# Optimization experiments

Measured on AMD Instinct MI355X. Metric: run time of the kernel, lower is better.

The kernel has to match this reference:

```python
import jax, jax.numpy as jnp
import numpy as np

S, B, E, H = 2048, 2, 1024, 16
D = E // H  # head dim = 64


def setup_inputs() -> dict:
    key = jax.random.key(0)
    k1, k2, k3 = jax.random.split(key, 3)
    x = jax.random.normal(k1, (S, B, E), dtype=jnp.float32)
    Wqkv = jax.random.normal(k2, (3 * E, E), dtype=jnp.float32) * (E ** -0.5)
    bqkv = jax.random.normal(k3, (3 * E,), dtype=jnp.float32) * 0.02
    return {"x": x, "Wqkv": Wqkv, "bqkv": bqkv}


def reference(x, Wqkv, bqkv):
    s, b, e = x.shape
    h, d = H, E // H
    # fused QKV projection: [S,B,E] @ [E,3E] -> [S,B,3E]
    qkv = jnp.einsum('sbe,fe->sbf', x, Wqkv) + bqkv
    q, k, v = jnp.split(qkv, 3, axis=-1)
    q = q.reshape(s, b, h, d)
    k = k.reshape(s, b, h, d)
    v = v.reshape(s, b, h, d)
    scale = 1.0 / jnp.sqrt(jnp.asarray(d, dtype=x.dtype))
    # scores: [B,H,S,S]
    scores = jnp.einsum('sbhd,tbhd->bhst', q, k) * scale
    attn = jax.nn.softmax(scores, axis=-1)
    # context: [S,B,H,D] -> [S,B,E]
    ctx = jnp.einsum('bhst,tbhd->sbhd', attn, v)
    return ctx.reshape(s, b, e)
```

## Files before the change

### kernel.cpp

```cpp
#include <hip/hip_runtime.h>

constexpr int SEQ   = 2048;
constexpr int BATCH = 2;
constexpr int EMB   = 1024;
constexpr int NH    = 16;
constexpr int HDIM  = 64;
constexpr int MROWS = SEQ * BATCH;
constexpr int KDIM  = EMB;
constexpr int NCOLS = 3 * EMB;

typedef __bf16 bf16x8 __attribute__((ext_vector_type(8)));
typedef __bf16 bf16x4 __attribute__((ext_vector_type(4)));
typedef float  f32x4  __attribute__((ext_vector_type(4)));
typedef float  f32x16 __attribute__((ext_vector_type(16)));
typedef unsigned int u32;
typedef unsigned int u32x4 __attribute__((ext_vector_type(4)));

__device__ __forceinline__ u32 cvt_pk_bf16(float lo, float hi) {
  u32 r;
  asm("v_cvt_pk_bf16_f32 %0, %1, %2" : "=v"(r) : "v"(lo), "v"(hi));
  return r;
}
__device__ __forceinline__ void pl32_swap(u32& a, u32& b) {
  asm("v_permlane32_swap_b32 %0, %1" : "+v"(a), "+v"(b));
}

__global__ __launch_bounds__(256) void cvt_f32_bf16(
    const float* __restrict__ src, __bf16* __restrict__ dst, int n4) {
  int stride = gridDim.x * blockDim.x;
  for (int i = blockIdx.x * blockDim.x + threadIdx.x; i < n4; i += stride) {
    float4 v = reinterpret_cast<const float4*>(src)[i];
    bf16x4 o;
    o[0] = (__bf16)v.x; o[1] = (__bf16)v.y; o[2] = (__bf16)v.z; o[3] = (__bf16)v.w;
    reinterpret_cast<bf16x4*>(dst)[i] = o;
  }
}

__global__ __launch_bounds__(256) void qkv_gemm(
    const __bf16* __restrict__ Xb, const __bf16* __restrict__ Wb,
    const float* __restrict__ bqkv,
    __bf16* __restrict__ Qb, __bf16* __restrict__ Kb, __bf16* __restrict__ Vt) {
  __shared__ __attribute__((aligned(16))) __bf16 Al[128][40];
  __shared__ __attribute__((aligned(16))) __bf16 Bl[128][40];

  const int tid  = threadIdx.x;
  const int lane = tid & 63;
  const int w    = tid >> 6;
  const int wm   = w >> 1, wn = w & 1;
  const int m0   = blockIdx.y * 128;
  const int n0   = blockIdx.x * 128;

  f32x4 acc[4][4] = {};

  for (int kt = 0; kt < KDIM / 32; ++kt) {
    const int k0 = kt * 32;
#pragma unroll
    for (int i = 0; i < 2; ++i) {
      int u = tid + i * 256;
      int row = u >> 2, c = u & 3;
      *reinterpret_cast<bf16x8*>(&Al[row][c * 8]) =
          *reinterpret_cast<const bf16x8*>(&Xb[(size_t)(m0 + row) * KDIM + k0 + c * 8]);
      *reinterpret_cast<bf16x8*>(&Bl[row][c * 8]) =
          *reinterpret_cast<const bf16x8*>(&Wb[(size_t)(n0 + row) * KDIM + k0 + c * 8]);
    }
    __syncthreads();

    bf16x8 af[4], bfr[4];
#pragma unroll
    for (int i = 0; i < 4; ++i)
      af[i] = *reinterpret_cast<const bf16x8*>(&Al[wm * 64 + i * 16 + (lane & 15)][(lane >> 4) * 8]);
#pragma unroll
    for (int j = 0; j < 4; ++j)
      bfr[j] = *reinterpret_cast<const bf16x8*>(&Bl[wn * 64 + j * 16 + (lane & 15)][(lane >> 4) * 8]);
#pragma unroll
    for (int i = 0; i < 4; ++i)
#pragma unroll
      for (int j = 0; j < 4; ++j)
        acc[i][j] = __builtin_amdgcn_mfma_f32_16x16x32_bf16(af[i], bfr[j], acc[i][j], 0, 0, 0);
    __syncthreads();
  }

  const float QSCALE = 0.18033688011112042f;
#pragma unroll
  for (int j = 0; j < 4; ++j) {
    const int f    = n0 + wn * 64 + j * 16 + (lane & 15);
    const float bias = bqkv[f];
    const int sec  = f >> 10;
    const int hd   = f & 1023;
    const int h    = hd >> 6, d = hd & 63;
#pragma unroll
    for (int i = 0; i < 4; ++i) {
#pragma unroll
      for (int r = 0; r < 4; ++r) {
        const int mm = m0 + wm * 64 + i * 16 + (lane >> 4) * 4 + r;
        const int s_ = mm >> 1, b_ = mm & 1;
        const int bh = b_ * NH + h;
        const float val = acc[i][j][r] + bias;
        if (sec == 0) {
          Qb[((size_t)bh * SEQ + s_) * HDIM + d] = (__bf16)(val * QSCALE);
        } else if (sec == 1) {
          Kb[((size_t)bh * SEQ + s_) * HDIM + d] = (__bf16)val;
        } else {
          Vt[((size_t)bh * HDIM + d) * SEQ + s_] = (__bf16)val;
        }
      }
    }
  }
}

__global__ __launch_bounds__(512) void attn_fwd(
    const __bf16* __restrict__ Qb, const __bf16* __restrict__ Kb,
    const __bf16* __restrict__ Vt, float* __restrict__ out) {
  __shared__ __attribute__((aligned(16))) __bf16 lds[8192];
  __bf16* Kl = lds;
  __bf16* Vl = lds + 4096;

  const int tid  = threadIdx.x;
  const int lane = tid & 63;
  const int w    = tid >> 6;
  const int lq   = lane & 31;
  const int hi   = lane >> 5;
  const int bh   = blockIdx.y;
  const int b_   = bh >> 4, h = bh & 15;
  const int q0   = blockIdx.x * 256 + w * 32;

  const __bf16* Qp = Qb + (size_t)bh * SEQ * HDIM;
  const __bf16* Kp = Kb + (size_t)bh * SEQ * HDIM;
  const __bf16* Vp = Vt + (size_t)bh * HDIM * SEQ;

  bf16x8 qf[4];
#pragma unroll
  for (int ks = 0; ks < 4; ++ks)
    qf[ks] = *reinterpret_cast<const bf16x8*>(&Qp[(size_t)(q0 + lq) * HDIM + ks * 16 + hi * 8]);

  f32x16 acc0 = {}, acc1 = {};
  float m = -1e30f, l = 0.f;

  const int srow = tid >> 3;
  const int scol = (tid & 7) * 8;
  const int sidx = srow * 64 + (scol ^ ((srow & 7) << 3));

  for (int t0 = 0; t0 < SEQ; t0 += 64) {
    __syncthreads();
    *reinterpret_cast<bf16x8*>(&Kl[sidx]) =
        *reinterpret_cast<const bf16x8*>(&Kp[(size_t)(t0 + srow) * HDIM + scol]);
    *reinterpret_cast<bf16x8*>(&Vl[sidx]) =
        *reinterpret_cast<const bf16x8*>(&Vp[(size_t)srow * SEQ + t0 + scol]);
    __syncthreads();

    f32x16 S0 = {}, S1 = {};
#pragma unroll
    for (int ks = 0; ks < 4; ++ks) {
      const int colb = ks * 16 + hi * 8;
      bf16x8 k0 = *reinterpret_cast<const bf16x8*>(&Kl[lq * 64        + (colb ^ ((lq & 7) << 3))]);
      bf16x8 k1 = *reinterpret_cast<const bf16x8*>(&Kl[(32 + lq) * 64 + (colb ^ ((lq & 7) << 3))]);
      S0 = __builtin_amdgcn_mfma_f32_32x32x16_bf16(k0, qf[ks], S0, 0, 0, 0);
      S1 = __builtin_amdgcn_mfma_f32_32x32x16_bf16(k1, qf[ks], S1, 0, 0, 0);
    }

    float pmax = S0[0];
#pragma unroll
    for (int i = 1; i < 16; ++i) pmax = fmaxf(pmax, S0[i]);
#pragma unroll
    for (int i = 0; i < 16; ++i) pmax = fmaxf(pmax, S1[i]);
    pmax = fmaxf(pmax, __shfl_xor(pmax, 32));
    const float mnew  = fmaxf(m, pmax);
    const float alpha = __builtin_amdgcn_exp2f(m - mnew);
    m = mnew;
    float rs = 0.f;
#pragma unroll
    for (int i = 0; i < 16; ++i) { S0[i] = __builtin_amdgcn_exp2f(S0[i] - mnew); rs += S0[i]; }
#pragma unroll
    for (int i = 0; i < 16; ++i) { S1[i] = __builtin_amdgcn_exp2f(S1[i] - mnew); rs += S1[i]; }
    l = l * alpha + rs;
#pragma unroll
    for (int i = 0; i < 16; ++i) { acc0[i] *= alpha; acc1[i] *= alpha; }

    bf16x8 pw[4];
    {
      auto mk = [&](const f32x16& P, bf16x8* dst) {
#pragma unroll
        for (int kk = 0; kk < 2; ++kk) {
          u32 a0 = cvt_pk_bf16(P[kk * 8 + 0], P[kk * 8 + 1]);
          u32 b0 = cvt_pk_bf16(P[kk * 8 + 4], P[kk * 8 + 5]);
          u32 a1 = cvt_pk_bf16(P[kk * 8 + 2], P[kk * 8 + 3]);
          u32 b1 = cvt_pk_bf16(P[kk * 8 + 6], P[kk * 8 + 7]);
          pl32_swap(a0, b0);
          pl32_swap(a1, b1);
          u32x4 wv; wv[0] = a0; wv[1] = a1; wv[2] = b0; wv[3] = b1;
          dst[kk] = __builtin_bit_cast(bf16x8, wv);
        }
      };
      mk(S0, &pw[0]);
      mk(S1, &pw[2]);
    }

#pragma unroll
    for (int ks = 0; ks < 4; ++ks) {
      const int colb = ks * 16 + hi * 8;
      bf16x8 v0 = *reinterpret_cast<const bf16x8*>(&Vl[lq * 64        + (colb ^ ((lq & 7) << 3))]);
      bf16x8 v1 = *reinterpret_cast<const bf16x8*>(&Vl[(32 + lq) * 64 + (colb ^ ((lq & 7) << 3))]);
      acc0 = __builtin_amdgcn_mfma_f32_32x32x16_bf16(v0, pw[ks], acc0, 0, 0, 0);
      acc1 = __builtin_amdgcn_mfma_f32_32x32x16_bf16(v1, pw[ks], acc1, 0, 0, 0);
    }
  }

  l += __shfl_xor(l, 32);
  const float inv = 1.0f / l;
  const int s_ = q0 + lq;
  float* op = out + ((size_t)s_ * BATCH + b_) * EMB + h * HDIM;
#pragma unroll
  for (int rr = 0; rr < 4; ++rr) {
    float4 o0 = {acc0[4 * rr] * inv, acc0[4 * rr + 1] * inv,
                 acc0[4 * rr + 2] * inv, acc0[4 * rr + 3] * inv};
    *reinterpret_cast<float4*>(&op[8 * rr + 4 * hi]) = o0;
    float4 o1 = {acc1[4 * rr] * inv, acc1[4 * rr + 1] * inv,
                 acc1[4 * rr + 2] * inv, acc1[4 * rr + 3] * inv};
    *reinterpret_cast<float4*>(&op[8 * rr + 4 * hi + 32]) = o1;
  }
}

extern "C" void kernel_launch(void* const* d_in, const int* in_sizes, int n_in,
                              void* d_out, int out_size, void* d_ws, size_t ws_size,
                              hipStream_t stream) {
  (void)in_sizes; (void)n_in; (void)out_size; (void)ws_size;
  const float* x    = (const float*)d_in[0];
  const float* Wqkv = (const float*)d_in[1];
  const float* bias = (const float*)d_in[2];
  float* out = (float*)d_out;

  char* ws = (char*)d_ws;
  __bf16* Xb = (__bf16*)(ws);
  __bf16* Wb = (__bf16*)(ws + 8388608);
  __bf16* Qb = (__bf16*)(ws + 14680064);
  __bf16* Kb = (__bf16*)(ws + 23068672);
  __bf16* Vt = (__bf16*)(ws + 31457280);

  cvt_f32_bf16<<<dim3(1024), dim3(256), 0, stream>>>(x, Xb, (MROWS * KDIM) / 4);
  cvt_f32_bf16<<<dim3(768), dim3(256), 0, stream>>>(Wqkv, Wb, (NCOLS * KDIM) / 4);
  qkv_gemm<<<dim3(NCOLS / 128, MROWS / 128), dim3(256), 0, stream>>>(Xb, Wb, bias, Qb, Kb, Vt);
  attn_fwd<<<dim3(SEQ / 256, BATCH * NH), dim3(512), 0, stream>>>(Qb, Kb, Vt, out);
}
```

Measured before the change: 117.5 us.

## Use direct global-to-LDS loads, double-buffer attention K/V, remap attention grid

The QKV GEMM now stages X and W tiles with global_load_lds into XOR-swizzled 64-wide K tiles, halving the number of loop iterations and barriers. The attention kernel double-buffers K/V tiles in LDS, prefetching the next tile with direct global-to-LDS loads while computing on the current one. It also switches to 256-thread blocks over a 1D grid of 512 workgroups with a remapped block-to-(head, query-tile) order. The aim is to hide global load latency and remove register round-trips. The cost is more LDS per block. The prefetch relies on a single barrier per iteration to order the async LDS writes, which is a correctness risk if the loads are not waited on.

New measurement: 126.1 us. +7.3%, slower.

```diff
diff --git a/kernel.cpp b/kernel.cpp
--- a/kernel.cpp
+++ b/kernel.cpp
@@ -24,6 +24,11 @@
 __device__ __forceinline__ void pl32_swap(u32& a, u32& b) {
   asm("v_permlane32_swap_b32 %0, %1" : "+v"(a), "+v"(b));
 }
+__device__ __forceinline__ void g2l16(const __bf16* g, __bf16* l) {
+  __builtin_amdgcn_global_load_lds(
+      (const __attribute__((address_space(1))) void*)g,
+      (__attribute__((address_space(3))) void*)l, 16, 0, 0);
+}
 
 __global__ __launch_bounds__(256) void cvt_f32_bf16(
     const float* __restrict__ src, __bf16* __restrict__ dst, int n4) {
@@ -40,8 +45,8 @@
     const __bf16* __restrict__ Xb, const __bf16* __restrict__ Wb,
     const float* __restrict__ bqkv,
     __bf16* __restrict__ Qb, __bf16* __restrict__ Kb, __bf16* __restrict__ Vt) {
-  __shared__ __attribute__((aligned(16))) __bf16 Al[128][40];
-  __shared__ __attribute__((aligned(16))) __bf16 Bl[128][40];
+  __shared__ __attribute__((aligned(16))) __bf16 Al[128 * 64];
+  __shared__ __attribute__((aligned(16))) __bf16 Bl[128 * 64];
 
   const int tid  = threadIdx.x;
   const int lane = tid & 63;
@@ -52,32 +57,36 @@
 
   f32x4 acc[4][4] = {};
 
-  for (int kt = 0; kt < KDIM / 32; ++kt) {
-    const int k0 = kt * 32;
-#pragma unroll
-    for (int i = 0; i < 2; ++i) {
-      int u = tid + i * 256;
-      int row = u >> 2, c = u & 3;
-      *reinterpret_cast<bf16x8*>(&Al[row][c * 8]) =
-          *reinterpret_cast<const bf16x8*>(&Xb[(size_t)(m0 + row) * KDIM + k0 + c * 8]);
-      *reinterpret_cast<bf16x8*>(&Bl[row][c * 8]) =
-          *reinterpret_cast<const bf16x8*>(&Wb[(size_t)(n0 + row) * KDIM + k0 + c * 8]);
-    }
+  for (int kt = 0; kt < KDIM / 64; ++kt) {
+    const int k0 = kt * 64;
     __syncthreads();
-
-    bf16x8 af[4], bfr[4];
-#pragma unroll
-    for (int i = 0; i < 4; ++i)
-      af[i] = *reinterpret_cast<const bf16x8*>(&Al[wm * 64 + i * 16 + (lane & 15)][(lane >> 4) * 8]);
-#pragma unroll
-    for (int j = 0; j < 4; ++j)
-      bfr[j] = *reinterpret_cast<const bf16x8*>(&Bl[wn * 64 + j * 16 + (lane & 15)][(lane >> 4) * 8]);
-#pragma unroll
-    for (int i = 0; i < 4; ++i)
-#pragma unroll
-      for (int j = 0; j < 4; ++j)
-        acc[i][j] = __builtin_amdgcn_mfma_f32_16x16x32_bf16(af[i], bfr[j], acc[i][j], 0, 0, 0);
+#pragma unroll
+    for (int c = 0; c < 4; ++c) {
+      const int u   = (w * 4 + c) * 64 + lane;
+      const int row = u >> 3;
+      const int sc  = ((u & 7) * 8) ^ ((row & 7) << 3);
+      g2l16(&Xb[(size_t)(m0 + row) * KDIM + k0 + sc], Al + (w * 4 + c) * 512);
+      g2l16(&Wb[(size_t)(n0 + row) * KDIM + k0 + sc], Bl + (w * 4 + c) * 512);
+    }
     __syncthreads();
+
+#pragma unroll
+    for (int s = 0; s < 2; ++s) {
+      bf16x8 af[4], bfr[4];
+#pragma unroll
+      for (int i = 0; i < 4; ++i) {
+        const int ra = wm * 64 + i * 16 + (lane & 15);
+        const int rb = wn * 64 + i * 16 + (lane & 15);
+        const int colb = s * 32 + (lane >> 4) * 8;
+        af[i]  = *reinterpret_cast<const bf16x8*>(&Al[ra * 64 + (colb ^ ((ra & 7) << 3))]);
+        bfr[i] = *reinterpret_cast<const bf16x8*>(&Bl[rb * 64 + (colb ^ ((rb & 7) << 3))]);
+      }
+#pragma unroll
+      for (int i = 0; i < 4; ++i)
+#pragma unroll
+        for (int j = 0; j < 4; ++j)
+          acc[i][j] = __builtin_amdgcn_mfma_f32_16x16x32_bf16(af[i], bfr[j], acc[i][j], 0, 0, 0);
+    }
   }
 
   const float QSCALE = 0.18033688011112042f;
@@ -108,21 +117,23 @@
   }
 }
 
-__global__ __launch_bounds__(512) void attn_fwd(
+__global__ __launch_bounds__(256) void attn_fwd(
     const __bf16* __restrict__ Qb, const __bf16* __restrict__ Kb,
     const __bf16* __restrict__ Vt, float* __restrict__ out) {
-  __shared__ __attribute__((aligned(16))) __bf16 lds[8192];
-  __bf16* Kl = lds;
-  __bf16* Vl = lds + 4096;
+  __shared__ __attribute__((aligned(16))) __bf16 lds[16384];
 
   const int tid  = threadIdx.x;
   const int lane = tid & 63;
   const int w    = tid >> 6;
   const int lq   = lane & 31;
   const int hi   = lane >> 5;
-  const int bh   = blockIdx.y;
+
+  const int bid  = blockIdx.x;
+  const int wgid = (bid & 7) * 64 + (bid >> 3);
+  const int qi   = wgid & 15;
+  const int bh   = wgid >> 4;
   const int b_   = bh >> 4, h = bh & 15;
-  const int q0   = blockIdx.x * 256 + w * 32;
+  const int q0   = qi * 128 + w * 32;
 
   const __bf16* Qp = Qb + (size_t)bh * SEQ * HDIM;
   const __bf16* Kp = Kb + (size_t)bh * SEQ * HDIM;
@@ -136,24 +147,32 @@
   f32x16 acc0 = {}, acc1 = {};
   float m = -1e30f, l = 0.f;
 
-  const int srow = tid >> 3;
-  const int scol = (tid & 7) * 8;
-  const int sidx = srow * 64 + (scol ^ ((srow & 7) << 3));
+  auto stage = [&](int b, int t0) {
+#pragma unroll
+    for (int c = 0; c < 2; ++c) {
+      const int u   = (w * 2 + c) * 64 + lane;
+      const int row = u >> 3;
+      const int sc  = ((u & 7) * 8) ^ ((row & 7) << 3);
+      g2l16(Kp + (size_t)(t0 + row) * HDIM + sc, lds + b * 8192 + (w * 2 + c) * 512);
+      g2l16(Vp + (size_t)row * SEQ + t0 + sc,    lds + b * 8192 + 4096 + (w * 2 + c) * 512);
+    }
+  };
+
+  stage(0, 0);
+  __syncthreads();
+  int cur = 0;
 
   for (int t0 = 0; t0 < SEQ; t0 += 64) {
-    __syncthreads();
-    *reinterpret_cast<bf16x8*>(&Kl[sidx]) =
-        *reinterpret_cast<const bf16x8*>(&Kp[(size_t)(t0 + srow) * HDIM + scol]);
-    *reinterpret_cast<bf16x8*>(&Vl[sidx]) =
-        *reinterpret_cast<const bf16x8*>(&Vp[(size_t)srow * SEQ + t0 + scol]);
-    __syncthreads();
+    if (t0 + 64 < SEQ) stage(cur ^ 1, t0 + 64);
+    const __bf16* kb = lds + cur * 8192;
+    const __bf16* vb = kb + 4096;
 
     f32x16 S0 = {}, S1 = {};
 #pragma unroll
     for (int ks = 0; ks < 4; ++ks) {
       const int colb = ks * 16 + hi * 8;
-      bf16x8 k0 = *reinterpret_cast<const bf16x8*>(&Kl[lq * 64        + (colb ^ ((lq & 7) << 3))]);
-      bf16x8 k1 = *reinterpret_cast<const bf16x8*>(&Kl[(32 + lq) * 64 + (colb ^ ((lq & 7) << 3))]);
+      bf16x8 k0 = *reinterpret_cast<const bf16x8*>(&kb[lq * 64        + (colb ^ ((lq & 7) << 3))]);
+      bf16x8 k1 = *reinterpret_cast<const bf16x8*>(&kb[(32 + lq) * 64 + (colb ^ ((lq & 7) << 3))]);
       S0 = __builtin_amdgcn_mfma_f32_32x32x16_bf16(k0, qf[ks], S0, 0, 0, 0);
       S1 = __builtin_amdgcn_mfma_f32_32x32x16_bf16(k1, qf[ks], S1, 0, 0, 0);
     }
@@ -198,11 +217,14 @@
 #pragma unroll
     for (int ks = 0; ks < 4; ++ks) {
       const int colb = ks * 16 + hi * 8;
-      bf16x8 v0 = *reinterpret_cast<const bf16x8*>(&Vl[lq * 64        + (colb ^ ((lq & 7) << 3))]);
-      bf16x8 v1 = *reinterpret_cast<const bf16x8*>(&Vl[(32 + lq) * 64 + (colb ^ ((lq & 7) << 3))]);
+      bf16x8 v0 = *reinterpret_cast<const bf16x8*>(&vb[lq * 64        + (colb ^ ((lq & 7) << 3))]);
+      bf16x8 v1 = *reinterpret_cast<const bf16x8*>(&vb[(32 + lq) * 64 + (colb ^ ((lq & 7) << 3))]);
       acc0 = __builtin_amdgcn_mfma_f32_32x32x16_bf16(v0, pw[ks], acc0, 0, 0, 0);
       acc1 = __builtin_amdgcn_mfma_f32_32x32x16_bf16(v1, pw[ks], acc1, 0, 0, 0);
     }
+
+    __syncthreads();
+    cur ^= 1;
   }
 
   l += __shfl_xor(l, 32);
@@ -239,5 +261,5 @@
   cvt_f32_bf16<<<dim3(1024), dim3(256), 0, stream>>>(x, Xb, (MROWS * KDIM) / 4);
   cvt_f32_bf16<<<dim3(768), dim3(256), 0, stream>>>(Wqkv, Wb, (NCOLS * KDIM) / 4);
   qkv_gemm<<<dim3(NCOLS / 128, MROWS / 128), dim3(256), 0, stream>>>(Xb, Wb, bias, Qb, Kb, Vt);
-  attn_fwd<<<dim3(SEQ / 256, BATCH * NH), dim3(512), 0, stream>>>(Qb, Kb, Vt, out);
-}
+  attn_fwd<<<dim3(512), dim3(256), 0, stream>>>(Qb, Kb, Vt, out);
+}
```
